# Kernel tuning notes

Measured on AMD Instinct MI355X. Metric: run time of the kernel, lower is better.

## Reference

```python
import jax, jax.numpy as jnp
import numpy as np
import math

H = 16
SEG = 128
DIL = 2


def hilbert_perm(M: int) -> jnp.ndarray:
    # Boustrophedon (snake) traversal of a ceil(sqrt(M)) grid, matching
    # create_hilbert_mapping_simple: skip linear positions >= M, keep first M.
    g = int(math.ceil(math.sqrt(M)))
    grid = np.arange(g * g).reshape(g, g)
    grid[1::2] = grid[1::2, ::-1]
    flat = grid.reshape(-1)
    flat = flat[flat < M][:M]
    return jnp.asarray(flat, dtype=jnp.int32)


def setup_inputs() -> dict:
    key = jax.random.key(0)
    kx, kq, ko = jax.random.split(key, 3)
    B, M, D = 4, 4096, 1024
    x = jax.random.normal(kx, (B, M, D), dtype=jnp.float32)
    # nn.Linear weights: [out_features, in_features], y = x @ W.T
    w_qkv = jax.random.normal(kq, (3 * D, D), dtype=jnp.float32) * (D ** -0.5)
    w_out = jax.random.normal(ko, (D, D), dtype=jnp.float32) * (D ** -0.5)
    return {"x": x, "w_qkv": w_qkv, "w_out": w_out}


def reference(x, w_qkv, w_out):
    B, M, Dm = x.shape
    hd = Dm // H
    scale = hd ** -0.5
    S = M // SEG  # number of segments (M chosen as a multiple of SEG)

    qkv = x @ w_qkv.T                              # [B, M, 3*Dm]
    qkv = qkv.reshape(B, M, 3, H, hd)
    q = qkv[:, :, 0].transpose(0, 2, 1, 3)         # [B, H, M, hd]
    k = qkv[:, :, 1].transpose(0, 2, 1, 3)
    v = qkv[:, :, 2].transpose(0, 2, 1, 3)

    perm = hilbert_perm(M)
    qh = q[:, :, perm]                             # Hilbert-reordered
    kh = k[:, :, perm]
    vh = v[:, :, perm]

    # segment-local dilated attention: each query attends to keys at
    # positions seg_start + j*DIL within its own segment
    qh = qh.reshape(B, H, S, SEG, hd)
    kd = kh.reshape(B, H, S, SEG, hd)[:, :, :, ::DIL]   # [B,H,S,SEG//DIL,hd]
    vd = vh.reshape(B, H, S, SEG, hd)[:, :, :, ::DIL]

    scores = jnp.einsum('bhsqd,bhskd->bhsqk', qh * scale, kd)
    attn = jax.nn.softmax(scores, axis=-1)
    o = jnp.einsum('bhsqk,bhskd->bhsqd', attn, vd)       # [B,H,S,SEG,hd]
    o = o.reshape(B, H, M, hd).transpose(0, 2, 1, 3).reshape(B, M, Dm)
    return o @ w_out.T
```

## Files before the change

### kernel.cpp

```cpp
#include <hip/hip_runtime.h>


typedef _Float16 f16x8 __attribute__((ext_vector_type(8)));
typedef _Float16 f16x4 __attribute__((ext_vector_type(4)));
typedef float f32x4 __attribute__((ext_vector_type(4)));

__device__ __forceinline__ int hperm(int i) {
  int r = i >> 6, c = i & 63;
  return (r << 6) | ((r & 1) ? (63 - c) : c);
}

__device__ __forceinline__ int arow_gather(int mp) {
  int b = mp >> 11, i = mp & 2047;
  int s = i >> 6, j = i & 63;
  return b * 4096 + hperm(s * 128 + 2 * j);
}

__device__ __forceinline__ void gload_lds16(const _Float16* g, _Float16* l) {
  __builtin_amdgcn_global_load_lds(
      (const __attribute__((address_space(1))) void*)g,
      (__attribute__((address_space(3))) void*)l, 16, 0, 0);
}

__global__ __launch_bounds__(256) void cast_all(
    const float* __restrict__ x, _Float16* __restrict__ xh,
    const float* __restrict__ wq, _Float16* __restrict__ wqh,
    const float* __restrict__ wo, _Float16* __restrict__ woh) {
  int i = blockIdx.x * 256 + threadIdx.x;
  const float* s;
  _Float16* d;
  int j;
  if (i < 4194304) {
    s = x; d = xh; j = i;
  } else if (i < 4194304 + 786432) {
    s = wq; d = wqh; j = i - 4194304;
  } else {
    s = wo; d = woh; j = i - (4194304 + 786432);
  }
  float4 v = ((const float4*)s)[j];
  f16x4 o;
  o[0] = (_Float16)v.x;
  o[1] = (_Float16)v.y;
  o[2] = (_Float16)v.z;
  o[3] = (_Float16)v.w;
  *(f16x4*)&d[(size_t)j * 4] = o;
}


#define BAR __builtin_amdgcn_s_barrier()
#define LGKM0                                          \
  do {                                                 \
    asm volatile("s_waitcnt lgkmcnt(0)" ::: "memory"); \
    __builtin_amdgcn_sched_barrier(0);                 \
  } while (0)
#define LGKM8 asm volatile("s_waitcnt lgkmcnt(8)" ::: "memory")
#define VM4 asm volatile("s_waitcnt vmcnt(4)" ::: "memory")
#define VM0 asm volatile("s_waitcnt vmcnt(0)" ::: "memory")

#define STG(mat, kt, h, buf)                                                 \
  do {                                                                       \
    const _Float16* g0 = ((mat) ? gpB : gpA)[(h)*2] + (size_t)(kt)*64;       \
    const _Float16* g1 = ((mat) ? gpB : gpA)[(h)*2 + 1] + (size_t)(kt)*64;   \
    _Float16* d_ = &lds[buf][mat][h][t * 8];                                 \
    gload_lds16(g0, d_);                                                     \
    gload_lds16(g1, d_ + 4096);                                              \
  } while (0)

#define LDA_(buf, mh)                                            \
  _Pragma("unroll") for (int m = 0; m < 4; m++) {                \
    a[0][m] = *(const f16x8*)(aB[buf][0] + (mh)*4096 + m * 1024); \
    a[1][m] = *(const f16x8*)(aB[buf][1] + (mh)*4096 + m * 1024); \
  }

#define LDB_(buf, nh)                                                   \
  _Pragma("unroll") for (int nf = 0; nf < 2; nf++) {                    \
    b[nh][0][nf] = *(const f16x8*)(bB[buf][0] + (nh)*2048 + nf * 1024); \
    b[nh][1][nf] = *(const f16x8*)(bB[buf][1] + (nh)*2048 + nf * 1024); \
  }

#define MM_(mh, nh)                                                        \
  __builtin_amdgcn_s_setprio(1);                                           \
  _Pragma("unroll") for (int m = 0; m < 4; m++)                            \
      _Pragma("unroll") for (int nf = 0; nf < 2; nf++)                     \
          _Pragma("unroll") for (int ks = 0; ks < 2; ks++) acc[(mh)*4 + m] \
              [(nh)*2 + nf] = __builtin_amdgcn_mfma_f32_16x16x32_f16(      \
                  a[ks][m], b[nh][ks][nf], acc[(mh)*4 + m][(nh)*2 + nf],   \
                  0, 0, 0);                                                \
  __builtin_amdgcn_s_setprio(0);

template <typename OutT>
__device__ __forceinline__ void gemm_body(
    const _Float16* const* gpA, const _Float16* const* gpB,
    OutT* __restrict__ C, int N, size_t arow0, size_t brow0,
    _Float16 (&lds)[2][2][2][8192]) {
  const int t = threadIdx.x;
  const int lane = t & 63, wave = t >> 6;
  const int wm = wave >> 2, wn = wave & 3;
  const int lr = lane & 15, lg = lane >> 4;

  const int cx0 = (lg * 8) ^ ((lr & 7) << 3);
  const int cx1 = cx0 ^ 32;
  const _Float16* aB[2][2];
  const _Float16* bB[2][2];
#pragma unroll
  for (int bf = 0; bf < 2; bf++) {
    aB[bf][0] = &lds[bf][0][wm][lr * 64 + cx0];
    aB[bf][1] = &lds[bf][0][wm][lr * 64 + cx1];
    bB[bf][0] = &lds[bf][1][wn >> 1][(wn & 1) * 4096 + lr * 64 + cx0];
    bB[bf][1] = &lds[bf][1][wn >> 1][(wn & 1) * 4096 + lr * 64 + cx1];
  }

  f32x4 acc[8][4] = {};
  f16x8 a[2][4], b[2][2][2];

  STG(0, 0, 0, 0);
  STG(0, 0, 1, 0);
  STG(1, 0, 0, 0);
  STG(1, 0, 1, 0);
  STG(1, 1, 0, 1);
  STG(1, 1, 1, 1);
  VM4;
  BAR;

  for (int i = 0; i < 7; i++) {
    const int k1 = 2 * i + 1, k2 = 2 * i + 2, k3 = 2 * i + 3;
    LDA_(0, 0); LDB_(0, 0); STG(0, k1, 0, 1); LGKM8; BAR; LGKM0; MM_(0, 0); BAR;
    LDB_(0, 1);             STG(0, k1, 1, 1);        BAR; LGKM0; MM_(0, 1); BAR;
    LDA_(0, 1);             STG(1, k2, 0, 0);        BAR; LGKM0; MM_(1, 1); BAR;
                            STG(1, k2, 1, 0); VM4;   BAR; LGKM0; MM_(1, 0); BAR;
    LDA_(1, 0); LDB_(1, 0); STG(0, k2, 0, 0); LGKM8; BAR; LGKM0; MM_(0, 0); BAR;
    LDB_(1, 1);             STG(0, k2, 1, 0);        BAR; LGKM0; MM_(0, 1); BAR;
    LDA_(1, 1);             STG(1, k3, 0, 1);        BAR; LGKM0; MM_(1, 1); BAR;
                            STG(1, k3, 1, 1); VM4;   BAR; LGKM0; MM_(1, 0); BAR;
  }

  {
    LDA_(0, 0); LDB_(0, 0); STG(0, 15, 0, 1); LGKM8; BAR; LGKM0; MM_(0, 0); BAR;
    LDB_(0, 1);             STG(0, 15, 1, 1);        BAR; LGKM0; MM_(0, 1); BAR;
    LDA_(0, 1);                                      BAR; LGKM0; MM_(1, 1); BAR;
                                              VM0;   BAR; LGKM0; MM_(1, 0); BAR;
    LDA_(1, 0); LDB_(1, 0);                          BAR; LGKM0; MM_(0, 0); BAR;
    LDB_(1, 1);                                      BAR; LGKM0; MM_(0, 1); BAR;
    LDA_(1, 1);                                      BAR; LGKM0; MM_(1, 1); BAR;
                                                          LGKM0; MM_(1, 0);
  }

#pragma unroll
  for (int mf = 0; mf < 8; mf++) {
    size_t row0 = arow0 + wm * 128 + mf * 16 + lg * 4;
#pragma unroll
    for (int nf = 0; nf < 4; nf++) {
      size_t col = brow0 + wn * 64 + nf * 16 + lr;
#pragma unroll
      for (int j = 0; j < 4; j++)
        C[(row0 + j) * N + col] = (OutT)acc[mf][nf][j];
    }
  }
}

__global__ __launch_bounds__(512, 2) void gemm_qkv8(
    const _Float16* __restrict__ xh, const _Float16* __restrict__ wqh,
    _Float16* __restrict__ qh, _Float16* __restrict__ kvh) {
  __shared__ _Float16 lds[2][2][2][8192];
  const int t = threadIdx.x;
  const int id = blockIdx.x;
  const int sw = (id & 7) * (gridDim.x >> 3) + (id >> 3);
  const bool iskv = sw >= 256;
  const int wid = iskv ? sw - 256 : sw;
  const int N = iskv ? 2048 : 1024;
  const int bn = iskv ? (wid & 7) : (wid & 3);
  const int bm = iskv ? (wid >> 3) : (wid >> 2);
  const _Float16* Bw = wqh + (iskv ? (size_t)1048576 : 0);
  _Float16* C = iskv ? kvh : qh;

  const int sgrow = t >> 3;
  const int sgcol = ((t & 7) * 8) ^ ((sgrow & 7) << 3);
  const _Float16* gpA[4];
  const _Float16* gpB[4];
#pragma unroll
  for (int r = 0; r < 4; r++) {
    int mr = bm * 256 + 64 * r + sgrow;
    int ar = iskv ? arow_gather(mr) : mr;
    gpA[r] = xh + (size_t)ar * 1024 + sgcol;
    gpB[r] = Bw + ((size_t)bn * 256 + 64 * r + sgrow) * 1024 + sgcol;
  }
  gemm_body<_Float16>(gpA, gpB, C, N, (size_t)bm * 256, (size_t)bn * 256, lds);
}

__global__ __launch_bounds__(512, 2) void gemm_out8(
    const _Float16* __restrict__ atth, const _Float16* __restrict__ woh,
    float* __restrict__ out) {
  __shared__ _Float16 lds[2][2][2][8192];
  const int t = threadIdx.x;
  const int id = blockIdx.x;
  const int sw = (id & 7) * (gridDim.x >> 3) + (id >> 3);
  const int bn = sw & 3, bm = sw >> 2;

  const int sgrow = t >> 3;
  const int sgcol = ((t & 7) * 8) ^ ((sgrow & 7) << 3);
  const _Float16* gpA[4];
  const _Float16* gpB[4];
#pragma unroll
  for (int r = 0; r < 4; r++) {
    gpA[r] = atth + ((size_t)bm * 256 + 64 * r + sgrow) * 1024 + sgcol;
    gpB[r] = woh + ((size_t)bn * 256 + 64 * r + sgrow) * 1024 + sgcol;
  }
  gemm_body<float>(gpA, gpB, out, 1024, (size_t)bm * 256, (size_t)bn * 256,
                   lds);
}

#define STRD 72

__global__ __launch_bounds__(256) void hilbert_attn(
    const _Float16* __restrict__ qh, const _Float16* __restrict__ kvh,
    _Float16* __restrict__ aout) {
  __shared__ _Float16 Qs[128 * STRD];
  __shared__ _Float16 Ks[64 * STRD];
  __shared__ _Float16 Vt[64 * STRD];
  __shared__ _Float16 Ps[128 * STRD];
  const int blk = blockIdx.x;
  const int s = blk & 31, h = (blk >> 5) & 15, b = blk >> 9;
  const int t = threadIdx.x, lane = t & 63, wave = t >> 6;
  const int lr = lane & 15, lg = lane >> 4, lk = lg * 8;
  const int col = (t & 7) * 8, rr = t >> 3;
  const size_t kvb = ((size_t)b * 2048 + s * 64) * 2048;

#pragma unroll
  for (int i = 0; i < 4; i++) {
    int m = i * 32 + rr;
    int p = b * 4096 + hperm(s * 128 + m);
    *(f16x8*)&Qs[m * STRD + col] =
        *(const f16x8*)&qh[(size_t)p * 1024 + h * 64 + col];
  }
#pragma unroll
  for (int i = 0; i < 2; i++) {
    int j = i * 32 + rr;
    *(f16x8*)&Ks[j * STRD + col] =
        *(const f16x8*)&kvh[kvb + (size_t)j * 2048 + h * 64 + col];
    f16x8 vv =
        *(const f16x8*)&kvh[kvb + (size_t)j * 2048 + 1024 + h * 64 + col];
#pragma unroll
    for (int e = 0; e < 8; e++) Vt[(col + e) * STRD + j] = vv[e];
  }
  __syncthreads();

  f32x4 accs[2][4] = {};
#pragma unroll
  for (int kk = 0; kk < 2; kk++) {
    f16x8 aa[2], bb[4];
#pragma unroll
    for (int m = 0; m < 2; m++)
      aa[m] = *(const f16x8*)&Qs[(wave * 32 + m * 16 + lr) * STRD + kk * 32 + lk];
#pragma unroll
    for (int n = 0; n < 4; n++)
      bb[n] = *(const f16x8*)&Ks[(n * 16 + lr) * STRD + kk * 32 + lk];
#pragma unroll
    for (int m = 0; m < 2; m++)
#pragma unroll
      for (int n = 0; n < 4; n++)
        accs[m][n] =
            __builtin_amdgcn_mfma_f32_16x16x32_f16(aa[m], bb[n], accs[m][n], 0, 0, 0);
  }

#pragma unroll
  for (int m = 0; m < 2; m++) {
#pragma unroll
    for (int j = 0; j < 4; j++) {
      float sc0 = accs[m][0][j] * 0.125f;
      float sc1 = accs[m][1][j] * 0.125f;
      float sc2 = accs[m][2][j] * 0.125f;
      float sc3 = accs[m][3][j] * 0.125f;
      float mx = fmaxf(fmaxf(sc0, sc1), fmaxf(sc2, sc3));
#pragma unroll
      for (int d = 1; d < 16; d <<= 1) mx = fmaxf(mx, __shfl_xor(mx, d, 16));
      float e0 = __expf(sc0 - mx), e1 = __expf(sc1 - mx);
      float e2 = __expf(sc2 - mx), e3 = __expf(sc3 - mx);
      float sum = (e0 + e1) + (e2 + e3);
#pragma unroll
      for (int d = 1; d < 16; d <<= 1) sum += __shfl_xor(sum, d, 16);
      float inv = 1.0f / sum;
      int row = wave * 32 + m * 16 + lg * 4 + j;
      Ps[row * STRD + 0 * 16 + lr] = (_Float16)(e0 * inv);
      Ps[row * STRD + 1 * 16 + lr] = (_Float16)(e1 * inv);
      Ps[row * STRD + 2 * 16 + lr] = (_Float16)(e2 * inv);
      Ps[row * STRD + 3 * 16 + lr] = (_Float16)(e3 * inv);
    }
  }
  __syncthreads();

  f32x4 acco[2][4] = {};
#pragma unroll
  for (int kk = 0; kk < 2; kk++) {
    f16x8 aa[2], bb[4];
#pragma unroll
    for (int m = 0; m < 2; m++)
      aa[m] = *(const f16x8*)&Ps[(wave * 32 + m * 16 + lr) * STRD + kk * 32 + lk];
#pragma unroll
    for (int n = 0; n < 4; n++)
      bb[n] = *(const f16x8*)&Vt[(n * 16 + lr) * STRD + kk * 32 + lk];
#pragma unroll
    for (int m = 0; m < 2; m++)
#pragma unroll
      for (int n = 0; n < 4; n++)
        acco[m][n] =
            __builtin_amdgcn_mfma_f32_16x16x32_f16(aa[m], bb[n], acco[m][n], 0, 0, 0);
  }

  const size_t orow0 = (size_t)b * 4096 + s * 128;
#pragma unroll
  for (int m = 0; m < 2; m++) {
#pragma unroll
    for (int n = 0; n < 4; n++) {
#pragma unroll
      for (int j = 0; j < 4; j++) {
        size_t row = orow0 + wave * 32 + m * 16 + lg * 4 + j;
        aout[row * 1024 + h * 64 + n * 16 + lr] = (_Float16)acco[m][n][j];
      }
    }
  }
}

extern "C" void kernel_launch(void* const* d_in, const int* in_sizes, int n_in,
                              void* d_out, int out_size, void* d_ws, size_t ws_size,
                              hipStream_t stream) {
  const float* x = (const float*)d_in[0];
  const float* w_qkv = (const float*)d_in[1];
  const float* w_out = (const float*)d_in[2];
  float* out = (float*)d_out;
  char* ws = (char*)d_ws;

  _Float16* xh = (_Float16*)(ws + 0);
  _Float16* wqh = (_Float16*)(ws + (size_t)33554432);
  _Float16* woh = (_Float16*)(ws + (size_t)39845888);
  _Float16* qh = (_Float16*)(ws + (size_t)41943040);
  _Float16* kvh = (_Float16*)(ws + (size_t)75497472);
  _Float16* atth = (_Float16*)(ws + (size_t)109051904);

  cast_all<<<20480, 256, 0, stream>>>(x, xh, w_qkv, wqh, w_out, woh);

  gemm_qkv8<<<512, 512, 0, stream>>>(xh, wqh, qh, kvh);
  hilbert_attn<<<2048, 256, 0, stream>>>(qh, kvh, atth);
  gemm_out8<<<256, 512, 0, stream>>>(atth, woh, out);
}
```

Measured before the change: 161.2 us.

## Shrink GEMM block tiles to 256x128 and restructure LDS pipeline

Both GEMMs move from 256x256 block tiles to 256x128, which doubles the grid to 1024 and 512 blocks and splits the 8 waves 4x2 into 64x64 warp tiles. The LDS layout becomes three 8K slabs per buffer (A halves plus B). A rewritten grouped schedule prefetches the next B fragment before the last MFMA quarter. The aim is better CU occupancy and wave balance on the smaller out-projection GEMM and fewer stalls. The cost is lower arithmetic intensity per block and more global traffic for A.

```diff
diff --git a/kernel.cpp b/kernel.cpp
--- a/kernel.cpp
+++ b/kernel.cpp
@@ -53,159 +53,189 @@
     asm volatile("s_waitcnt lgkmcnt(0)" ::: "memory"); \
     __builtin_amdgcn_sched_barrier(0);                 \
   } while (0)
-#define LGKM8 asm volatile("s_waitcnt lgkmcnt(8)" ::: "memory")
-#define VM4 asm volatile("s_waitcnt vmcnt(4)" ::: "memory")
+#define VM2 asm volatile("s_waitcnt vmcnt(2)" ::: "memory")
 #define VM0 asm volatile("s_waitcnt vmcnt(0)" ::: "memory")
 
-#define STG(mat, kt, h, buf)                                                 \
-  do {                                                                       \
-    const _Float16* g0 = ((mat) ? gpB : gpA)[(h)*2] + (size_t)(kt)*64;       \
-    const _Float16* g1 = ((mat) ? gpB : gpA)[(h)*2 + 1] + (size_t)(kt)*64;   \
-    _Float16* d_ = &lds[buf][mat][h][t * 8];                                 \
-    gload_lds16(g0, d_);                                                     \
-    gload_lds16(g1, d_ + 4096);                                              \
-  } while (0)
-
-#define LDA_(buf, mh)                                            \
-  _Pragma("unroll") for (int m = 0; m < 4; m++) {                \
-    a[0][m] = *(const f16x8*)(aB[buf][0] + (mh)*4096 + m * 1024); \
-    a[1][m] = *(const f16x8*)(aB[buf][1] + (mh)*4096 + m * 1024); \
-  }
-
-#define LDB_(buf, nh)                                                   \
-  _Pragma("unroll") for (int nf = 0; nf < 2; nf++) {                    \
-    b[nh][0][nf] = *(const f16x8*)(bB[buf][0] + (nh)*2048 + nf * 1024); \
-    b[nh][1][nf] = *(const f16x8*)(bB[buf][1] + (nh)*2048 + nf * 1024); \
-  }
-
-#define MM_(mh, nh)                                                        \
-  __builtin_amdgcn_s_setprio(1);                                           \
-  _Pragma("unroll") for (int m = 0; m < 4; m++)                            \
-      _Pragma("unroll") for (int nf = 0; nf < 2; nf++)                     \
-          _Pragma("unroll") for (int ks = 0; ks < 2; ks++) acc[(mh)*4 + m] \
-              [(nh)*2 + nf] = __builtin_amdgcn_mfma_f32_16x16x32_f16(      \
-                  a[ks][m], b[nh][ks][nf], acc[(mh)*4 + m][(nh)*2 + nf],   \
-                  0, 0, 0);                                                \
+#define STG_A0(kt, bf)                                        \
+  do {                                                        \
+    gload_lds16(gpA[0] + (kt)*64, &lds[bf][0][t * 8]);        \
+    gload_lds16(gpA[1] + (kt)*64, &lds[bf][0][t * 8 + 4096]); \
+  } while (0)
+#define STG_A1(kt, bf)                                        \
+  do {                                                        \
+    gload_lds16(gpA[2] + (kt)*64, &lds[bf][1][t * 8]);        \
+    gload_lds16(gpA[3] + (kt)*64, &lds[bf][1][t * 8 + 4096]); \
+  } while (0)
+#define STG_B(kt, bf)                                         \
+  do {                                                        \
+    gload_lds16(gpB[0] + (kt)*64, &lds[bf][2][t * 8]);        \
+    gload_lds16(gpB[1] + (kt)*64, &lds[bf][2][t * 8 + 4096]); \
+  } while (0)
+
+#define LDA0(bf)                                                        \
+  _Pragma("unroll") for (int ks = 0; ks < 2; ks++)                      \
+      _Pragma("unroll") for (int m = 0; m < 2; m++) aA0[ks][m] =        \
+          *(const f16x8*)(aBase[bf][ks] + m * 1024);
+#define LDA1(bf)                                                        \
+  _Pragma("unroll") for (int ks = 0; ks < 2; ks++)                      \
+      _Pragma("unroll") for (int m = 0; m < 2; m++) aA1[ks][m] =        \
+          *(const f16x8*)(aBase[bf][ks] + 2048 + m * 1024);
+#define LDB1(bf)                                                        \
+  _Pragma("unroll") for (int ks = 0; ks < 2; ks++)                      \
+      _Pragma("unroll") for (int nf = 0; nf < 2; nf++) bB1[ks][nf] =    \
+          *(const f16x8*)(bBase[bf][ks] + 2048 + nf * 1024);
+#define LDB0(bf, par)                                                   \
+  _Pragma("unroll") for (int ks = 0; ks < 2; ks++)                      \
+      _Pragma("unroll") for (int nf = 0; nf < 2; nf++) bB0g[par][ks][nf] = \
+          *(const f16x8*)(bBase[bf][ks] + nf * 1024);
+
+#define MMQ(ACCR, ACCC, AARR, BARR)                                          \
+  __builtin_amdgcn_s_setprio(1);                                             \
+  _Pragma("unroll") for (int m = 0; m < 2; m++)                              \
+      _Pragma("unroll") for (int nf = 0; nf < 2; nf++)                       \
+          _Pragma("unroll") for (int ks = 0; ks < 2; ks++)                   \
+              acc[(ACCR) + m][(ACCC) + nf] =                                 \
+                  __builtin_amdgcn_mfma_f32_16x16x32_f16(                    \
+                      AARR[ks][m], BARR[ks][nf], acc[(ACCR) + m][(ACCC) + nf], \
+                      0, 0, 0);                                              \
   __builtin_amdgcn_s_setprio(0);
 
+#define MM00(P) MMQ(0, 0, aA0, bB0g[P])
+#define MM01() MMQ(0, 2, aA0, bB1)
+#define MM11() MMQ(2, 2, aA1, bB1)
+#define MM10(P) MMQ(2, 0, aA1, bB0g[P])
+
+#define GROUP(P, kt1, kt2, SA, SB, VMN, PRE)        \
+  do {                                              \
+                                            \
+    LDA0(P);                                        \
+    if (SA) { STG_A0(kt1, (P) ^ 1); }               \
+    BAR; LGKM0; MM00(P); BAR;                       \
+                                            \
+    LDB1(P);                                        \
+    if (SA) { STG_A1(kt1, (P) ^ 1); }               \
+    BAR; LGKM0; MM01(); BAR;                        \
+                                            \
+    LDA1(P);                                        \
+    if (SB) { STG_B(kt2, P); }                      \
+    BAR; LGKM0; MM11(); BAR;                        \
+                                            \
+    if ((VMN) == 2) { VM2; }                        \
+    else if ((VMN) == 0) { VM0; }                   \
+    BAR;                                            \
+    __builtin_amdgcn_sched_barrier(0);              \
+    if (PRE) { LDB0((P) ^ 1, (P) ^ 1); }            \
+    MM10(P); BAR;                                   \
+  } while (0)
+
 template <typename OutT>
-__device__ __forceinline__ void gemm_body(
-    const _Float16* const* gpA, const _Float16* const* gpB,
-    OutT* __restrict__ C, int N, size_t arow0, size_t brow0,
-    _Float16 (&lds)[2][2][2][8192]) {
+__device__ __forceinline__ void gemm_body(const _Float16* const* gpA,
+                                          const _Float16* const* gpB,
+                                          OutT* __restrict__ C, int N,
+                                          size_t arow0, size_t bcol0,
+                                          _Float16 (&lds)[2][3][8192]) {
   const int t = threadIdx.x;
   const int lane = t & 63, wave = t >> 6;
-  const int wm = wave >> 2, wn = wave & 3;
+  const int wm = wave >> 1, wn = wave & 1;
   const int lr = lane & 15, lg = lane >> 4;
 
   const int cx0 = (lg * 8) ^ ((lr & 7) << 3);
   const int cx1 = cx0 ^ 32;
-  const _Float16* aB[2][2];
-  const _Float16* bB[2][2];
+  const _Float16* aBase[2][2];
+  const _Float16* bBase[2][2];
 #pragma unroll
   for (int bf = 0; bf < 2; bf++) {
-    aB[bf][0] = &lds[bf][0][wm][lr * 64 + cx0];
-    aB[bf][1] = &lds[bf][0][wm][lr * 64 + cx1];
-    bB[bf][0] = &lds[bf][1][wn >> 1][(wn & 1) * 4096 + lr * 64 + cx0];
-    bB[bf][1] = &lds[bf][1][wn >> 1][(wn & 1) * 4096 + lr * 64 + cx1];
-  }
-
-  f32x4 acc[8][4] = {};
-  f16x8 a[2][4], b[2][2][2];
-
-  STG(0, 0, 0, 0);
-  STG(0, 0, 1, 0);
-  STG(1, 0, 0, 0);
-  STG(1, 0, 1, 0);
-  STG(1, 1, 0, 1);
-  STG(1, 1, 1, 1);
-  VM4;
+    aBase[bf][0] = &lds[bf][wm >> 1][((wm & 1) * 64 + lr) * 64 + cx0];
+    aBase[bf][1] = &lds[bf][wm >> 1][((wm & 1) * 64 + lr) * 64 + cx1];
+    bBase[bf][0] = &lds[bf][2][(wn * 64 + lr) * 64 + cx0];
+    bBase[bf][1] = &lds[bf][2][(wn * 64 + lr) * 64 + cx1];
+  }
+
+  f32x4 acc[4][4] = {};
+  f16x8 aA0[2][2], aA1[2][2], bB1[2][2], bB0g[2][2][2];
+
+  STG_A0(0, 0);
+  STG_A1(0, 0);
+  STG_B(0, 0);
+  STG_B(1, 1);
+  VM2;
   BAR;
+  __builtin_amdgcn_sched_barrier(0);
+  LDB0(0, 0);
 
   for (int i = 0; i < 7; i++) {
-    const int k1 = 2 * i + 1, k2 = 2 * i + 2, k3 = 2 * i + 3;
-    LDA_(0, 0); LDB_(0, 0); STG(0, k1, 0, 1); LGKM8; BAR; LGKM0; MM_(0, 0); BAR;
-    LDB_(0, 1);             STG(0, k1, 1, 1);        BAR; LGKM0; MM_(0, 1); BAR;
-    LDA_(0, 1);             STG(1, k2, 0, 0);        BAR; LGKM0; MM_(1, 1); BAR;
-                            STG(1, k2, 1, 0); VM4;   BAR; LGKM0; MM_(1, 0); BAR;
-    LDA_(1, 0); LDB_(1, 0); STG(0, k2, 0, 0); LGKM8; BAR; LGKM0; MM_(0, 0); BAR;
-    LDB_(1, 1);             STG(0, k2, 1, 0);        BAR; LGKM0; MM_(0, 1); BAR;
-    LDA_(1, 1);             STG(1, k3, 0, 1);        BAR; LGKM0; MM_(1, 1); BAR;
-                            STG(1, k3, 1, 1); VM4;   BAR; LGKM0; MM_(1, 0); BAR;
-  }
-
-  {
-    LDA_(0, 0); LDB_(0, 0); STG(0, 15, 0, 1); LGKM8; BAR; LGKM0; MM_(0, 0); BAR;
-    LDB_(0, 1);             STG(0, 15, 1, 1);        BAR; LGKM0; MM_(0, 1); BAR;
-    LDA_(0, 1);                                      BAR; LGKM0; MM_(1, 1); BAR;
-                                              VM0;   BAR; LGKM0; MM_(1, 0); BAR;
-    LDA_(1, 0); LDB_(1, 0);                          BAR; LGKM0; MM_(0, 0); BAR;
-    LDB_(1, 1);                                      BAR; LGKM0; MM_(0, 1); BAR;
-    LDA_(1, 1);                                      BAR; LGKM0; MM_(1, 1); BAR;
-                                                          LGKM0; MM_(1, 0);
-  }
-
-#pragma unroll
-  for (int mf = 0; mf < 8; mf++) {
-    size_t row0 = arow0 + wm * 128 + mf * 16 + lg * 4;
-#pragma unroll
-    for (int nf = 0; nf < 4; nf++) {
-      size_t col = brow0 + wn * 64 + nf * 16 + lr;
+    GROUP(0, 2 * i + 1, 2 * i + 2, 1, 1, 2, 1);
+    GROUP(1, 2 * i + 2, 2 * i + 3, 1, 1, 2, 1);
+  }
+  GROUP(0, 15, 0, 1, 0, 0, 1);
+  GROUP(1, 0, 0, 0, 0, -1, 0);
+
+#pragma unroll
+  for (int mi = 0; mi < 4; mi++) {
+    size_t row0 = arow0 + wm * 64 + mi * 16 + lg * 4;
+#pragma unroll
+    for (int ni = 0; ni < 4; ni++) {
+      size_t col = bcol0 + wn * 64 + ni * 16 + lr;
 #pragma unroll
       for (int j = 0; j < 4; j++)
-        C[(row0 + j) * N + col] = (OutT)acc[mf][nf][j];
+        C[(row0 + j) * N + col] = (OutT)acc[mi][ni][j];
     }
   }
 }
 
-__global__ __launch_bounds__(512, 2) void gemm_qkv8(
+__global__ __launch_bounds__(512, 2) void gemm_qkv(
     const _Float16* __restrict__ xh, const _Float16* __restrict__ wqh,
     _Float16* __restrict__ qh, _Float16* __restrict__ kvh) {
-  __shared__ _Float16 lds[2][2][2][8192];
+  __shared__ _Float16 lds[2][3][8192];
   const int t = threadIdx.x;
   const int id = blockIdx.x;
   const int sw = (id & 7) * (gridDim.x >> 3) + (id >> 3);
-  const bool iskv = sw >= 256;
-  const int wid = iskv ? sw - 256 : sw;
+  const bool iskv = sw >= 512;
+  const int wid = sw & 511;
   const int N = iskv ? 2048 : 1024;
-  const int bn = iskv ? (wid & 7) : (wid & 3);
-  const int bm = iskv ? (wid >> 3) : (wid >> 2);
+  const int bn = iskv ? (wid & 15) : (wid & 7);
+  const int bm = iskv ? (wid >> 4) : (wid >> 3);
   const _Float16* Bw = wqh + (iskv ? (size_t)1048576 : 0);
   _Float16* C = iskv ? kvh : qh;
 
   const int sgrow = t >> 3;
   const int sgcol = ((t & 7) * 8) ^ ((sgrow & 7) << 3);
   const _Float16* gpA[4];
-  const _Float16* gpB[4];
+  const _Float16* gpB[2];
 #pragma unroll
   for (int r = 0; r < 4; r++) {
     int mr = bm * 256 + 64 * r + sgrow;
     int ar = iskv ? arow_gather(mr) : mr;
     gpA[r] = xh + (size_t)ar * 1024 + sgcol;
-    gpB[r] = Bw + ((size_t)bn * 256 + 64 * r + sgrow) * 1024 + sgcol;
-  }
-  gemm_body<_Float16>(gpA, gpB, C, N, (size_t)bm * 256, (size_t)bn * 256, lds);
-}
-
-__global__ __launch_bounds__(512, 2) void gemm_out8(
+  }
+#pragma unroll
+  for (int r = 0; r < 2; r++)
+    gpB[r] = Bw + ((size_t)bn * 128 + 64 * r + sgrow) * 1024 + sgcol;
+
+  gemm_body<_Float16>(gpA, gpB, C, N, (size_t)bm * 256, (size_t)bn * 128, lds);
+}
+
+__global__ __launch_bounds__(512, 2) void gemm_out(
     const _Float16* __restrict__ atth, const _Float16* __restrict__ woh,
     float* __restrict__ out) {
-  __shared__ _Float16 lds[2][2][2][8192];
+  __shared__ _Float16 lds[2][3][8192];
   const int t = threadIdx.x;
   const int id = blockIdx.x;
   const int sw = (id & 7) * (gridDim.x >> 3) + (id >> 3);
-  const int bn = sw & 3, bm = sw >> 2;
+  const int bn = sw & 7, bm = sw >> 3;
 
   const int sgrow = t >> 3;
   const int sgcol = ((t & 7) * 8) ^ ((sgrow & 7) << 3);
   const _Float16* gpA[4];
-  const _Float16* gpB[4];
-#pragma unroll
-  for (int r = 0; r < 4; r++) {
+  const _Float16* gpB[2];
+#pragma unroll
+  for (int r = 0; r < 4; r++)
     gpA[r] = atth + ((size_t)bm * 256 + 64 * r + sgrow) * 1024 + sgcol;
-    gpB[r] = woh + ((size_t)bn * 256 + 64 * r + sgrow) * 1024 + sgcol;
-  }
-  gemm_body<float>(gpA, gpB, out, 1024, (size_t)bm * 256, (size_t)bn * 256,
+#pragma unroll
+  for (int r = 0; r < 2; r++)
+    gpB[r] = woh + ((size_t)bn * 128 + 64 * r + sgrow) * 1024 + sgcol;
+
+  gemm_body<float>(gpA, gpB, out, 1024, (size_t)bm * 256, (size_t)bn * 128,
                    lds);
 }
 
@@ -338,7 +368,7 @@
 
   cast_all<<<20480, 256, 0, stream>>>(x, xh, w_qkv, wqh, w_out, woh);
 
-  gemm_qkv8<<<512, 512, 0, stream>>>(xh, wqh, qh, kvh);
+  gemm_qkv<<<1024, 512, 0, stream>>>(xh, wqh, qh, kvh);
   hilbert_attn<<<2048, 256, 0, stream>>>(qh, kvh, atth);
-  gemm_out8<<<256, 512, 0, stream>>>(atth, woh, out);
-}
+  gemm_out<<<512, 512, 0, stream>>>(atth, woh, out);
+}
```

New measurement: 174.6 us. +8.3%, slower.
